# Kernel tuning notes

Measured on AMD Instinct MI355X. Metric: run time of the kernel, lower is better.

Reference implementation:

```python
import jax, jax.numpy as jnp
from jax import lax
import numpy as np

CH = 512      # ch_in = c_in = c_out
P = 8         # p: channels per group
NG = CH // P  # depthwise groups
PG = CH // P  # pointwise groups
EPS = 1e-5
DN = ('NCHW', 'OIHW', 'NCHW')


def leaky(x):
    return jnp.where(x >= 0, x, 0.01 * x)  # LeakyReLU default slope


def setup_inputs() -> dict:
    key = jax.random.key(0)
    ks = jax.random.split(key, 8)
    N, H, W = 16, 64, 64
    return {
        'style_encoding': jax.random.normal(ks[0], (N, 512, 4, 4), jnp.float32),
        'content_in': jax.random.normal(ks[1], (N, CH, H, W), jnp.float32),
        'dw_w': jax.random.normal(ks[2], (P, 512, 2, 2), jnp.float32) * 0.05,
        'dw_b': jax.random.normal(ks[3], (P,), jnp.float32) * 0.05,
        'pk_w': jax.random.normal(ks[4], (P, 512), jnp.float32) * 0.05,
        'pk_b': jax.random.normal(ks[5], (P,), jnp.float32) * 0.05,
        'pb_w': jax.random.normal(ks[6], (CH, 512), jnp.float32) * 0.05,
        'pb_b': jax.random.normal(ks[7], (CH,), jnp.float32) * 0.05,
    }


def reference(style_encoding, content_in, dw_w, dw_b, pk_w, pk_b, pb_w, pb_b):
    N, _, H, W = content_in.shape
    # --- KernelPredictor ---
    # depthwise kernels: 2x2 valid conv on 4x4 style map -> [N, P, 3, 3]
    d = lax.conv_general_dilated(style_encoding, dw_w, (1, 1), 'VALID',
                                 dimension_numbers=DN)
    d = leaky(d + dw_b[None, :, None, None])  # [N, P, 3, 3]
    # expand: same [P,3,3] filter for every output channel -> [N, CH, P, 3, 3]
    depthwise = jnp.broadcast_to(d[:, None], (N, CH, P, 3, 3))
    # avg-pool 4 on 4x4 style map == global mean -> [N, 512]
    s_d = jnp.mean(style_encoding, axis=(2, 3))
    pk = jnp.einsum('nc,oc->no', s_d, pk_w) + pk_b       # [N, P]  (1x1 conv)
    bias = jnp.einsum('nc,oc->no', s_d, pb_w) + pb_b     # [N, CH] (1x1 conv)

    # --- per-sample grouped convs, batched by folding batch into groups ---
    padded = jnp.pad(content_in, ((0, 0), (0, 0), (1, 1), (1, 1)), mode='reflect')
    xr = padded.reshape(1, N * CH, H + 2, W + 2)
    wr = depthwise.reshape(N * CH, P, 3, 3)
    depth = lax.conv_general_dilated(xr, wr, (1, 1), 'VALID',
                                     feature_group_count=N * NG,
                                     dimension_numbers=DN)
    depth = depth.reshape(N, CH, H, W)

    # pointwise 1x1 grouped conv: weight [N, CH, P, 1, 1], identical over out
    # channels within a sample (expand); groups = PG, CH//PG == P out ch/group
    depth_g = depth.reshape(N, PG, P, H, W)
    pw_g = jnp.broadcast_to(pk[:, None, None, :], (N, PG, P, P))  # [n,g,o,j]
    out = jnp.einsum('ngjhw,ngoj->ngohw', depth_g, pw_g).reshape(N, CH, H, W)
    predicted = leaky(out + bias[:, :, None, None])

    # --- instance-norm of content (AdaIN calc_mean_std, unbiased var) ---
    mean = jnp.mean(content_in, axis=(2, 3), keepdims=True)
    std = jnp.sqrt(jnp.var(content_in, axis=(2, 3), keepdims=True, ddof=1) + EPS)
    normalized = (content_in - mean) / std
    return normalized * predicted
```

## Files before the change

### kernel.cpp

```cpp
#include <hip/hip_runtime.h>
#include <math.h>

#define CH 512
#define P 8
#define PLANE 4096
#define EPS 1e-5f

__device__ __forceinline__ float leaky(float x) { return x >= 0.f ? x : 0.01f * x; }

__device__ __forceinline__ float wave_sum(float v) {
    #pragma unroll
    for (int off = 32; off; off >>= 1) v += __shfl_xor(v, off, 64);
    return v;
}

__global__ __launch_bounds__(64) void sd_pk_kernel(
    const float* __restrict__ style,
    const float* __restrict__ pk_w,
    const float* __restrict__ pk_b,
    float* __restrict__ sd_out,
    float* __restrict__ S_out)
{
    const int n = blockIdx.x;
    const int lane = threadIdx.x;
    const float4* sp = (const float4*)(style + (size_t)n * 8192);
    float sd[8];
    #pragma unroll
    for (int i = 0; i < 8; ++i) {
        int c = lane + 64 * i;
        float4 a = sp[c * 4 + 0], b = sp[c * 4 + 1];
        float4 d = sp[c * 4 + 2], e = sp[c * 4 + 3];
        float s = a.x + a.y + a.z + a.w + b.x + b.y + b.z + b.w
                + d.x + d.y + d.z + d.w + e.x + e.y + e.z + e.w;
        sd[i] = s * (1.f / 16.f);
        sd_out[n * 512 + c] = sd[i];
    }
    float Ssum = 0.f;
    #pragma unroll
    for (int o = 0; o < 8; ++o) {
        float acc = 0.f;
        #pragma unroll
        for (int i = 0; i < 8; ++i)
            acc += pk_w[o * 512 + lane + 64 * i] * sd[i];
        Ssum += wave_sum(acc) + pk_b[o];
    }
    if (lane == 0) S_out[n] = Ssum;
}

__global__ __launch_bounds__(256) void dconv_kernel(
    const float* __restrict__ style,
    const float* __restrict__ dw_w,
    const float* __restrict__ dw_b,
    float* __restrict__ d_pred)
{
    const int W = blockIdx.x * 4 + (threadIdx.x >> 6);
    const int lane = threadIdx.x & 63;
    const int n = W / 72, r = W % 72;
    const int j = r / 9, pos = r % 9, y = pos / 3, x = pos % 3;
    const float* sb = style + (size_t)n * 8192;
    const float4* wp = (const float4*)dw_w;
    float acc = 0.f;
    #pragma unroll
    for (int i = 0; i < 8; ++i) {
        int c = lane + 64 * i;
        float4 w = wp[j * 512 + c];
        const float* s = sb + c * 16 + y * 4 + x;
        acc += s[0] * w.x + s[1] * w.y + s[4] * w.z + s[5] * w.w;
    }
    acc = wave_sum(acc);
    if (lane == 0) d_pred[n * 72 + r] = leaky(acc + dw_b[j]);
}

__global__ __launch_bounds__(256) void bias_kernel(
    const float* __restrict__ sd,
    const float* __restrict__ pb_w,
    const float* __restrict__ pb_b,
    float* __restrict__ bias_out)
{
    const int c = blockIdx.x * 4 + (threadIdx.x >> 6);
    const int lane = threadIdx.x & 63;
    float w[8];
    #pragma unroll
    for (int i = 0; i < 8; ++i) w[i] = pb_w[(size_t)c * 512 + lane + 64 * i];
    float acc[16];
    #pragma unroll
    for (int nn = 0; nn < 16; ++nn) acc[nn] = 0.f;
    #pragma unroll
    for (int i = 0; i < 8; ++i) {
        #pragma unroll
        for (int nn = 0; nn < 16; ++nn)
            acc[nn] += w[i] * sd[nn * 512 + lane + 64 * i];
    }
    #pragma unroll
    for (int nn = 0; nn < 16; ++nn) acc[nn] = wave_sum(acc[nn]);
    if (lane == 0) {
        float bb = pb_b[c];
        #pragma unroll
        for (int nn = 0; nn < 16; ++nn) bias_out[nn * 512 + c] = acc[nn] + bb;
    }
}

__global__ __launch_bounds__(256) void stats_kernel(
    const float* __restrict__ content,
    float* __restrict__ mean_out,
    float* __restrict__ rstd_out)
{
    const int nc = blockIdx.x;
    const int t = threadIdx.x;
    const float4* base = (const float4*)(content + (size_t)nc * PLANE);
    float s = 0.f, sq = 0.f;
    #pragma unroll
    for (int k = 0; k < 4; ++k) {
        float4 v = base[k * 256 + t];
        s  += v.x + v.y + v.z + v.w;
        sq += v.x * v.x + v.y * v.y + v.z * v.z + v.w * v.w;
    }
    #pragma unroll
    for (int off = 32; off > 0; off >>= 1) {
        s  += __shfl_down(s, off, 64);
        sq += __shfl_down(sq, off, 64);
    }
    __shared__ float ls[4], lq[4];
    const int wave = t >> 6, lane = t & 63;
    if (lane == 0) { ls[wave] = s; lq[wave] = sq; }
    __syncthreads();
    if (t == 0) {
        float S = ls[0] + ls[1] + ls[2] + ls[3];
        float Q = lq[0] + lq[1] + lq[2] + lq[3];
        float m = S * (1.f / 4096.f);
        float var = (Q - 4096.f * m * m) * (1.f / 4095.f);
        mean_out[nc] = m;
        rstd_out[nc] = rsqrtf(var + EPS);
    }
}

__global__ __launch_bounds__(256) void main_kernel(
    const float* __restrict__ content,
    const float* __restrict__ d_pred,
    const float* __restrict__ S_in,
    const float* __restrict__ bias_in,
    const float* __restrict__ mean_in,
    const float* __restrict__ rstd_in,
    float* __restrict__ out)
{
    const int b    = blockIdx.x;
    const int tile = b & 3;
    const int g    = (b >> 2) & 63;
    const int n    = b >> 8;
    const int t  = threadIdx.x;
    const int tx = t & 15, ty = t >> 4;
    const int h  = tile * 16 + ty;
    const int x0 = tx * 4;

    __shared__ float s_d[72];
    __shared__ float s_S;
    __shared__ float s_bias[8], s_mean[8], s_rstd[8];
    if (t < 72) s_d[t] = d_pred[n * 72 + t];
    if (t == 80) s_S = S_in[n];
    if (t >= 88 && t < 96) {
        int o = t - 88;
        int c = n * 512 + g * 8 + o;
        s_bias[o] = bias_in[c];
        s_mean[o] = mean_in[c];
        s_rstd[o] = rstd_in[c];
    }
    __syncthreads();

    const float* cbase = content + (size_t)(n * 512 + g * 8) * PLANE;
    float D0 = 0.f, D1 = 0.f, D2 = 0.f, D3 = 0.f;
    float4 xc[8];

    #pragma unroll
    for (int j = 0; j < 8; ++j) {
        const float* cj = cbase + j * PLANE;
        #pragma unroll
        for (int r = 0; r < 3; ++r) {
            int y = h - 1 + r;
            int ry = y < 0 ? 1 : (y > 63 ? 62 : y);
            float4 v = *(const float4*)(cj + ry * 64 + x0);
            float lv = __shfl_up(v.w, 1, 64);
            float rv = __shfl_down(v.x, 1, 64);
            float xm = (tx == 0)  ? v.y : lv;
            float xp = (tx == 15) ? v.z : rv;
            const float w0 = s_d[j * 9 + r * 3 + 0];
            const float w1 = s_d[j * 9 + r * 3 + 1];
            const float w2 = s_d[j * 9 + r * 3 + 2];
            D0 += w0 * xm  + w1 * v.x + w2 * v.y;
            D1 += w0 * v.x + w1 * v.y + w2 * v.z;
            D2 += w0 * v.y + w1 * v.z + w2 * v.w;
            D3 += w0 * v.z + w1 * v.w + w2 * xp;
            if (r == 1) xc[j] = v;
        }
    }

    const float S = s_S;
    const float P0 = D0 * S, P1 = D1 * S, P2 = D2 * S, P3 = D3 * S;
    float* obase = out + (size_t)(n * 512 + g * 8) * PLANE + h * 64 + x0;
    #pragma unroll
    for (int o = 0; o < 8; ++o) {
        float bb = s_bias[o], m = s_mean[o], rs = s_rstd[o];
        float4 res;
        res.x = (xc[o].x - m) * rs * leaky(P0 + bb);
        res.y = (xc[o].y - m) * rs * leaky(P1 + bb);
        res.z = (xc[o].z - m) * rs * leaky(P2 + bb);
        res.w = (xc[o].w - m) * rs * leaky(P3 + bb);
        *(float4*)(obase + o * PLANE) = res;
    }
}

extern "C" void kernel_launch(void* const* d_in, const int* in_sizes, int n_in,
                              void* d_out, int out_size, void* d_ws, size_t ws_size,
                              hipStream_t stream) {
    const float* style   = (const float*)d_in[0];
    const float* content = (const float*)d_in[1];
    const float* dw_w    = (const float*)d_in[2];
    const float* dw_b    = (const float*)d_in[3];
    const float* pk_w    = (const float*)d_in[4];
    const float* pk_b    = (const float*)d_in[5];
    const float* pb_w    = (const float*)d_in[6];
    const float* pb_b    = (const float*)d_in[7];
    float* out = (float*)d_out;
    float* ws  = (float*)d_ws;

    const int N = 16;
    float* sd_ws   = ws;
    float* d_pred  = sd_ws + N * 512;
    float* S_ws    = d_pred + N * 72;
    float* bias_ws = S_ws + N;
    float* mean_ws = bias_ws + N * 512;
    float* rstd_ws = mean_ws + N * 512;

    sd_pk_kernel<<<N, 64, 0, stream>>>(style, pk_w, pk_b, sd_ws, S_ws);
    dconv_kernel<<<N * 72 / 4, 256, 0, stream>>>(style, dw_w, dw_b, d_pred);
    bias_kernel<<<512 / 4, 256, 0, stream>>>(sd_ws, pb_w, pb_b, bias_ws);
    stats_kernel<<<N * 512, 256, 0, stream>>>(content, mean_ws, rstd_ws);
    main_kernel<<<N * 64 * 4, 256, 0, stream>>>(content, d_pred, S_ws, bias_ws,
                                                mean_ws, rstd_ws, out);
}
```

Baseline: 278.5 us.

## Fuse instance-norm stats and bias GEMV into main kernel, merge style kernels

After: 309.2 us. +11.0%, slower.

```diff
diff --git a/kernel.cpp b/kernel.cpp
--- a/kernel.cpp
+++ b/kernel.cpp
@@ -1,10 +1,10 @@
 #include <hip/hip_runtime.h>
 #include <math.h>
 
-#define CH 512
-#define P 8
 #define PLANE 4096
 #define EPS 1e-5f
+
+typedef float f4 __attribute__((ext_vector_type(4)));
 
 __device__ __forceinline__ float leaky(float x) { return x >= 0.f ? x : 0.01f * x; }
 
@@ -14,197 +14,176 @@
     return v;
 }
 
-__global__ __launch_bounds__(64) void sd_pk_kernel(
+__global__ __launch_bounds__(256) void style_kernel(
     const float* __restrict__ style,
+    const float* __restrict__ dw_w,
+    const float* __restrict__ dw_b,
     const float* __restrict__ pk_w,
     const float* __restrict__ pk_b,
     float* __restrict__ sd_out,
-    float* __restrict__ S_out)
-{
-    const int n = blockIdx.x;
-    const int lane = threadIdx.x;
-    const float4* sp = (const float4*)(style + (size_t)n * 8192);
-    float sd[8];
-    #pragma unroll
-    for (int i = 0; i < 8; ++i) {
-        int c = lane + 64 * i;
-        float4 a = sp[c * 4 + 0], b = sp[c * 4 + 1];
-        float4 d = sp[c * 4 + 2], e = sp[c * 4 + 3];
-        float s = a.x + a.y + a.z + a.w + b.x + b.y + b.z + b.w
-                + d.x + d.y + d.z + d.w + e.x + e.y + e.z + e.w;
-        sd[i] = s * (1.f / 16.f);
-        sd_out[n * 512 + c] = sd[i];
-    }
-    float Ssum = 0.f;
-    #pragma unroll
-    for (int o = 0; o < 8; ++o) {
-        float acc = 0.f;
-        #pragma unroll
-        for (int i = 0; i < 8; ++i)
-            acc += pk_w[o * 512 + lane + 64 * i] * sd[i];
-        Ssum += wave_sum(acc) + pk_b[o];
-    }
-    if (lane == 0) S_out[n] = Ssum;
-}
-
-__global__ __launch_bounds__(256) void dconv_kernel(
-    const float* __restrict__ style,
-    const float* __restrict__ dw_w,
-    const float* __restrict__ dw_b,
+    float* __restrict__ S_out,
     float* __restrict__ d_pred)
 {
-    const int W = blockIdx.x * 4 + (threadIdx.x >> 6);
-    const int lane = threadIdx.x & 63;
-    const int n = W / 72, r = W % 72;
-    const int j = r / 9, pos = r % 9, y = pos / 3, x = pos % 3;
+    const int blk = blockIdx.x;
+    const int n = blk & 15;
+    const int t = threadIdx.x;
+    const int wave = t >> 6, lane = t & 63;
     const float* sb = style + (size_t)n * 8192;
-    const float4* wp = (const float4*)dw_w;
-    float acc = 0.f;
-    #pragma unroll
-    for (int i = 0; i < 8; ++i) {
-        int c = lane + 64 * i;
-        float4 w = wp[j * 512 + c];
-        const float* s = sb + c * 16 + y * 4 + x;
-        acc += s[0] * w.x + s[1] * w.y + s[4] * w.z + s[5] * w.w;
-    }
-    acc = wave_sum(acc);
-    if (lane == 0) d_pred[n * 72 + r] = leaky(acc + dw_b[j]);
-}
-
-__global__ __launch_bounds__(256) void bias_kernel(
+
+    if (blk < 16) {
+        __shared__ float s_sd[512];
+        __shared__ float red[4];
+        #pragma unroll
+        for (int q = 0; q < 2; ++q) {
+            int c = t + 256 * q;
+            const float4* sp = (const float4*)sb + c * 4;
+            float4 a = sp[0], b = sp[1], d = sp[2], e = sp[3];
+            float s = a.x + a.y + a.z + a.w + b.x + b.y + b.z + b.w
+                    + d.x + d.y + d.z + d.w + e.x + e.y + e.z + e.w;
+            s *= (1.f / 16.f);
+            s_sd[c] = s;
+            sd_out[n * 512 + c] = s;
+        }
+        __syncthreads();
+        float part = 0.f;
+        #pragma unroll
+        for (int o = 0; o < 8; ++o)
+            part += pk_w[o * 512 + t] * s_sd[t]
+                  + pk_w[o * 512 + t + 256] * s_sd[t + 256];
+        part = wave_sum(part);
+        if (lane == 0) red[wave] = part;
+        __syncthreads();
+        if (t == 0) {
+            float S = red[0] + red[1] + red[2] + red[3];
+            #pragma unroll
+            for (int o = 0; o < 8; ++o) S += pk_b[o];
+            S_out[n] = S;
+        }
+    } else {
+        const float4* wp = (const float4*)dw_w;
+        for (int rr = 0; rr < 18; ++rr) {
+            int r = wave * 18 + rr;
+            int j = r / 9, pos = r % 9, y = pos / 3, x = pos % 3;
+            float acc = 0.f;
+            #pragma unroll
+            for (int i = 0; i < 8; ++i) {
+                int c = lane + 64 * i;
+                float4 w = wp[j * 512 + c];
+                const float* s = sb + c * 16 + y * 4 + x;
+                acc += s[0] * w.x + s[1] * w.y + s[4] * w.z + s[5] * w.w;
+            }
+            acc = wave_sum(acc);
+            if (lane == 0) d_pred[n * 72 + r] = leaky(acc + dw_b[j]);
+        }
+    }
+}
+
+__global__ __launch_bounds__(256) void fused_kernel(
+    const float* __restrict__ content,
+    const float* __restrict__ d_pred,
+    const float* __restrict__ S_in,
     const float* __restrict__ sd,
     const float* __restrict__ pb_w,
     const float* __restrict__ pb_b,
-    float* __restrict__ bias_out)
-{
-    const int c = blockIdx.x * 4 + (threadIdx.x >> 6);
-    const int lane = threadIdx.x & 63;
-    float w[8];
-    #pragma unroll
-    for (int i = 0; i < 8; ++i) w[i] = pb_w[(size_t)c * 512 + lane + 64 * i];
-    float acc[16];
-    #pragma unroll
-    for (int nn = 0; nn < 16; ++nn) acc[nn] = 0.f;
-    #pragma unroll
-    for (int i = 0; i < 8; ++i) {
-        #pragma unroll
-        for (int nn = 0; nn < 16; ++nn)
-            acc[nn] += w[i] * sd[nn * 512 + lane + 64 * i];
-    }
-    #pragma unroll
-    for (int nn = 0; nn < 16; ++nn) acc[nn] = wave_sum(acc[nn]);
-    if (lane == 0) {
-        float bb = pb_b[c];
-        #pragma unroll
-        for (int nn = 0; nn < 16; ++nn) bias_out[nn * 512 + c] = acc[nn] + bb;
-    }
-}
-
-__global__ __launch_bounds__(256) void stats_kernel(
-    const float* __restrict__ content,
-    float* __restrict__ mean_out,
-    float* __restrict__ rstd_out)
-{
-    const int nc = blockIdx.x;
-    const int t = threadIdx.x;
-    const float4* base = (const float4*)(content + (size_t)nc * PLANE);
-    float s = 0.f, sq = 0.f;
-    #pragma unroll
-    for (int k = 0; k < 4; ++k) {
-        float4 v = base[k * 256 + t];
-        s  += v.x + v.y + v.z + v.w;
-        sq += v.x * v.x + v.y * v.y + v.z * v.z + v.w * v.w;
-    }
-    #pragma unroll
-    for (int off = 32; off > 0; off >>= 1) {
-        s  += __shfl_down(s, off, 64);
-        sq += __shfl_down(sq, off, 64);
-    }
-    __shared__ float ls[4], lq[4];
-    const int wave = t >> 6, lane = t & 63;
-    if (lane == 0) { ls[wave] = s; lq[wave] = sq; }
-    __syncthreads();
-    if (t == 0) {
-        float S = ls[0] + ls[1] + ls[2] + ls[3];
-        float Q = lq[0] + lq[1] + lq[2] + lq[3];
-        float m = S * (1.f / 4096.f);
-        float var = (Q - 4096.f * m * m) * (1.f / 4095.f);
-        mean_out[nc] = m;
-        rstd_out[nc] = rsqrtf(var + EPS);
-    }
-}
-
-__global__ __launch_bounds__(256) void main_kernel(
-    const float* __restrict__ content,
-    const float* __restrict__ d_pred,
-    const float* __restrict__ S_in,
-    const float* __restrict__ bias_in,
-    const float* __restrict__ mean_in,
-    const float* __restrict__ rstd_in,
     float* __restrict__ out)
 {
-    const int b    = blockIdx.x;
-    const int tile = b & 3;
-    const int g    = (b >> 2) & 63;
-    const int n    = b >> 8;
-    const int t  = threadIdx.x;
+    const int b = blockIdx.x;
+    const int g = b & 63, n = b >> 6;
+    const int t = threadIdx.x;
     const int tx = t & 15, ty = t >> 4;
-    const int h  = tile * 16 + ty;
-    const int x0 = tx * 4;
+    const int wave = t >> 6, lane = t & 63;
 
     __shared__ float s_d[72];
     __shared__ float s_S;
     __shared__ float s_bias[8], s_mean[8], s_rstd[8];
+    __shared__ float reds[32], redq[32];
+
     if (t < 72) s_d[t] = d_pred[n * 72 + t];
     if (t == 80) s_S = S_in[n];
-    if (t >= 88 && t < 96) {
-        int o = t - 88;
-        int c = n * 512 + g * 8 + o;
-        s_bias[o] = bias_in[c];
-        s_mean[o] = mean_in[c];
-        s_rstd[o] = rstd_in[c];
-    }
-    __syncthreads();
+
+    {
+        const int o = t >> 5, l = t & 31;
+        const float* pw  = pb_w + (size_t)(g * 8 + o) * 512;
+        const float* sdn = sd + n * 512;
+        float acc = 0.f;
+        #pragma unroll
+        for (int i = 0; i < 16; ++i) acc += pw[l + 32 * i] * sdn[l + 32 * i];
+        #pragma unroll
+        for (int off = 16; off; off >>= 1) acc += __shfl_xor(acc, off, 64);
+        if (l == 0) s_bias[o] = acc + pb_b[g * 8 + o];
+    }
 
     const float* cbase = content + (size_t)(n * 512 + g * 8) * PLANE;
-    float D0 = 0.f, D1 = 0.f, D2 = 0.f, D3 = 0.f;
-    float4 xc[8];
 
     #pragma unroll
     for (int j = 0; j < 8; ++j) {
-        const float* cj = cbase + j * PLANE;
-        #pragma unroll
-        for (int r = 0; r < 3; ++r) {
-            int y = h - 1 + r;
-            int ry = y < 0 ? 1 : (y > 63 ? 62 : y);
-            float4 v = *(const float4*)(cj + ry * 64 + x0);
-            float lv = __shfl_up(v.w, 1, 64);
-            float rv = __shfl_down(v.x, 1, 64);
-            float xm = (tx == 0)  ? v.y : lv;
-            float xp = (tx == 15) ? v.z : rv;
-            const float w0 = s_d[j * 9 + r * 3 + 0];
-            const float w1 = s_d[j * 9 + r * 3 + 1];
-            const float w2 = s_d[j * 9 + r * 3 + 2];
-            D0 += w0 * xm  + w1 * v.x + w2 * v.y;
-            D1 += w0 * v.x + w1 * v.y + w2 * v.z;
-            D2 += w0 * v.y + w1 * v.z + w2 * v.w;
-            D3 += w0 * v.z + w1 * v.w + w2 * xp;
-            if (r == 1) xc[j] = v;
-        }
-    }
+        const float4* p = (const float4*)(cbase + j * PLANE);
+        float sm = 0.f, sq = 0.f;
+        #pragma unroll
+        for (int k = 0; k < 4; ++k) {
+            float4 v = p[k * 256 + t];
+            sm += v.x + v.y + v.z + v.w;
+            sq += v.x * v.x + v.y * v.y + v.z * v.z + v.w * v.w;
+        }
+        #pragma unroll
+        for (int off = 32; off; off >>= 1) {
+            sm += __shfl_xor(sm, off, 64);
+            sq += __shfl_xor(sq, off, 64);
+        }
+        if (lane == 0) { reds[j * 4 + wave] = sm; redq[j * 4 + wave] = sq; }
+    }
+    __syncthreads();
+    if (t < 8) {
+        float S4 = reds[t * 4] + reds[t * 4 + 1] + reds[t * 4 + 2] + reds[t * 4 + 3];
+        float Q4 = redq[t * 4] + redq[t * 4 + 1] + redq[t * 4 + 2] + redq[t * 4 + 3];
+        float m = S4 * (1.f / 4096.f);
+        float var = (Q4 - 4096.f * m * m) * (1.f / 4095.f);
+        s_mean[t] = m;
+        s_rstd[t] = rsqrtf(var + EPS);
+    }
+    __syncthreads();
 
     const float S = s_S;
-    const float P0 = D0 * S, P1 = D1 * S, P2 = D2 * S, P3 = D3 * S;
-    float* obase = out + (size_t)(n * 512 + g * 8) * PLANE + h * 64 + x0;
-    #pragma unroll
-    for (int o = 0; o < 8; ++o) {
-        float bb = s_bias[o], m = s_mean[o], rs = s_rstd[o];
-        float4 res;
-        res.x = (xc[o].x - m) * rs * leaky(P0 + bb);
-        res.y = (xc[o].y - m) * rs * leaky(P1 + bb);
-        res.z = (xc[o].z - m) * rs * leaky(P2 + bb);
-        res.w = (xc[o].w - m) * rs * leaky(P3 + bb);
-        *(float4*)(obase + o * PLANE) = res;
+    #pragma unroll 1
+    for (int k = 0; k < 4; ++k) {
+        const int h = k * 16 + ty;
+        const int x0 = tx * 4;
+        float D0 = 0.f, D1 = 0.f, D2 = 0.f, D3 = 0.f;
+        float4 xc[8];
+        #pragma unroll
+        for (int j = 0; j < 8; ++j) {
+            const float* cj = cbase + j * PLANE;
+            #pragma unroll
+            for (int r = 0; r < 3; ++r) {
+                int y = h - 1 + r;
+                int ry = y < 0 ? 1 : (y > 63 ? 62 : y);
+                float4 v = *(const float4*)(cj + ry * 64 + x0);
+                float lv = __shfl_up(v.w, 1, 64);
+                float rv = __shfl_down(v.x, 1, 64);
+                float xm = (tx == 0)  ? v.y : lv;
+                float xp = (tx == 15) ? v.z : rv;
+                const float w0 = s_d[j * 9 + r * 3 + 0];
+                const float w1 = s_d[j * 9 + r * 3 + 1];
+                const float w2 = s_d[j * 9 + r * 3 + 2];
+                D0 += w0 * xm  + w1 * v.x + w2 * v.y;
+                D1 += w0 * v.x + w1 * v.y + w2 * v.z;
+                D2 += w0 * v.y + w1 * v.z + w2 * v.w;
+                D3 += w0 * v.z + w1 * v.w + w2 * xp;
+                if (r == 1) xc[j] = v;
+            }
+        }
+        const float P0 = D0 * S, P1 = D1 * S, P2 = D2 * S, P3 = D3 * S;
+        float* obase = out + (size_t)(n * 512 + g * 8) * PLANE + h * 64 + x0;
+        #pragma unroll
+        for (int o = 0; o < 8; ++o) {
+            float bb = s_bias[o], m = s_mean[o], rs = s_rstd[o];
+            f4 res;
+            res.x = (xc[o].x - m) * rs * leaky(P0 + bb);
+            res.y = (xc[o].y - m) * rs * leaky(P1 + bb);
+            res.z = (xc[o].z - m) * rs * leaky(P2 + bb);
+            res.w = (xc[o].w - m) * rs * leaky(P3 + bb);
+            __builtin_nontemporal_store(res, (f4*)(obase + o * PLANE));
+        }
     }
 }
 
@@ -223,17 +202,12 @@
     float* ws  = (float*)d_ws;
 
     const int N = 16;
-    float* sd_ws   = ws;
-    float* d_pred  = sd_ws + N * 512;
-    float* S_ws    = d_pred + N * 72;
-    float* bias_ws = S_ws + N;
-    float* mean_ws = bias_ws + N * 512;
-    float* rstd_ws = mean_ws + N * 512;
-
-    sd_pk_kernel<<<N, 64, 0, stream>>>(style, pk_w, pk_b, sd_ws, S_ws);
-    dconv_kernel<<<N * 72 / 4, 256, 0, stream>>>(style, dw_w, dw_b, d_pred);
-    bias_kernel<<<512 / 4, 256, 0, stream>>>(sd_ws, pb_w, pb_b, bias_ws);
-    stats_kernel<<<N * 512, 256, 0, stream>>>(content, mean_ws, rstd_ws);
-    main_kernel<<<N * 64 * 4, 256, 0, stream>>>(content, d_pred, S_ws, bias_ws,
-                                                mean_ws, rstd_ws, out);
-}
+    float* sd_ws  = ws;
+    float* d_pred = sd_ws + N * 512;
+    float* S_ws   = d_pred + N * 72;
+
+    style_kernel<<<32, 256, 0, stream>>>(style, dw_w, dw_b, pk_w, pk_b,
+                                         sd_ws, S_ws, d_pred);
+    fused_kernel<<<N * 64, 256, 0, stream>>>(content, d_pred, S_ws, sd_ws,
+                                             pb_w, pb_b, out);
+}
```

## Stage content halo tiles in LDS in two four-channel phases

Applied to the files above, without the earlier changes.

Measured after the change: 353.6 us. 26.9% more time.

```diff
diff --git a/kernel.cpp b/kernel.cpp
--- a/kernel.cpp
+++ b/kernel.cpp
@@ -5,6 +5,12 @@
 #define P 8
 #define PLANE 4096
 #define EPS 1e-5f
+
+#define ROWS 18
+#define LDW  68
+#define LPLANE (ROWS * LDW)
+
+typedef float f4 __attribute__((ext_vector_type(4)));
 
 __device__ __forceinline__ float leaky(float x) { return x >= 0.f ? x : 0.01f * x; }
 
@@ -134,7 +140,7 @@
     }
 }
 
-__global__ __launch_bounds__(256) void main_kernel(
+__global__ __launch_bounds__(256, 6) void main_kernel(
     const float* __restrict__ content,
     const float* __restrict__ d_pred,
     const float* __restrict__ S_in,
@@ -152,9 +158,11 @@
     const int h  = tile * 16 + ty;
     const int x0 = tx * 4;
 
+    __shared__ float s_x[4 * LPLANE];
     __shared__ float s_d[72];
     __shared__ float s_S;
     __shared__ float s_bias[8], s_mean[8], s_rstd[8];
+
     if (t < 72) s_d[t] = d_pred[n * 72 + t];
     if (t == 80) s_S = S_in[n];
     if (t >= 88 && t < 96) {
@@ -164,24 +172,39 @@
         s_mean[o] = mean_in[c];
         s_rstd[o] = rstd_in[c];
     }
+
+    const float* cbase = content + (size_t)(n * 512 + g * 8) * PLANE;
+    const int xmi = (tx == 0)  ? 1  : x0 - 1;
+    const int xpi = (tx == 15) ? 62 : x0 + 4;
+
+    float D0 = 0.f, D1 = 0.f, D2 = 0.f, D3 = 0.f;
+    f4 xc0[4];
+
+    #pragma unroll
+    for (int i = 0; i < 5; ++i) {
+        int q = t + 256 * i;
+        if (q < 1152) {
+            int p   = q / 288;
+            int rem = q - p * 288;
+            int row = rem >> 4;
+            int c4  = rem & 15;
+            int y   = tile * 16 + row - 1;
+            int ry  = y < 0 ? 1 : (y > 63 ? 62 : y);
+            f4 v = *(const f4*)(cbase + p * PLANE + ry * 64 + c4 * 4);
+            *(f4*)(s_x + p * LPLANE + row * LDW + c4 * 4) = v;
+        }
+    }
     __syncthreads();
 
-    const float* cbase = content + (size_t)(n * 512 + g * 8) * PLANE;
-    float D0 = 0.f, D1 = 0.f, D2 = 0.f, D3 = 0.f;
-    float4 xc[8];
-
-    #pragma unroll
-    for (int j = 0; j < 8; ++j) {
-        const float* cj = cbase + j * PLANE;
+    #pragma unroll
+    for (int j = 0; j < 4; ++j) {
+        const float* base = s_x + j * LPLANE;
         #pragma unroll
         for (int r = 0; r < 3; ++r) {
-            int y = h - 1 + r;
-            int ry = y < 0 ? 1 : (y > 63 ? 62 : y);
-            float4 v = *(const float4*)(cj + ry * 64 + x0);
-            float lv = __shfl_up(v.w, 1, 64);
-            float rv = __shfl_down(v.x, 1, 64);
-            float xm = (tx == 0)  ? v.y : lv;
-            float xp = (tx == 15) ? v.z : rv;
+            const float* rowp = base + (ty + r) * LDW;
+            f4 v = *(const f4*)(rowp + x0);
+            float xm = rowp[xmi];
+            float xp = rowp[xpi];
             const float w0 = s_d[j * 9 + r * 3 + 0];
             const float w1 = s_d[j * 9 + r * 3 + 1];
             const float w2 = s_d[j * 9 + r * 3 + 2];
@@ -189,7 +212,43 @@
             D1 += w0 * v.x + w1 * v.y + w2 * v.z;
             D2 += w0 * v.y + w1 * v.z + w2 * v.w;
             D3 += w0 * v.z + w1 * v.w + w2 * xp;
-            if (r == 1) xc[j] = v;
+        }
+        xc0[j] = *(const f4*)(base + (ty + 1) * LDW + x0);
+    }
+    __syncthreads();
+
+    #pragma unroll
+    for (int i = 0; i < 5; ++i) {
+        int q = t + 256 * i;
+        if (q < 1152) {
+            int p   = q / 288;
+            int rem = q - p * 288;
+            int row = rem >> 4;
+            int c4  = rem & 15;
+            int y   = tile * 16 + row - 1;
+            int ry  = y < 0 ? 1 : (y > 63 ? 62 : y);
+            f4 v = *(const f4*)(cbase + (p + 4) * PLANE + ry * 64 + c4 * 4);
+            *(f4*)(s_x + p * LPLANE + row * LDW + c4 * 4) = v;
+        }
+    }
+    __syncthreads();
+
+    #pragma unroll
+    for (int j = 0; j < 4; ++j) {
+        const float* base = s_x + j * LPLANE;
+        #pragma unroll
+        for (int r = 0; r < 3; ++r) {
+            const float* rowp = base + (ty + r) * LDW;
+            f4 v = *(const f4*)(rowp + x0);
+            float xm = rowp[xmi];
+            float xp = rowp[xpi];
+            const float w0 = s_d[(j + 4) * 9 + r * 3 + 0];
+            const float w1 = s_d[(j + 4) * 9 + r * 3 + 1];
+            const float w2 = s_d[(j + 4) * 9 + r * 3 + 2];
+            D0 += w0 * xm  + w1 * v.x + w2 * v.y;
+            D1 += w0 * v.x + w1 * v.y + w2 * v.z;
+            D2 += w0 * v.y + w1 * v.z + w2 * v.w;
+            D3 += w0 * v.z + w1 * v.w + w2 * xp;
         }
     }
 
@@ -197,14 +256,26 @@
     const float P0 = D0 * S, P1 = D1 * S, P2 = D2 * S, P3 = D3 * S;
     float* obase = out + (size_t)(n * 512 + g * 8) * PLANE + h * 64 + x0;
     #pragma unroll
-    for (int o = 0; o < 8; ++o) {
+    for (int o = 0; o < 4; ++o) {
+        f4 v = xc0[o];
         float bb = s_bias[o], m = s_mean[o], rs = s_rstd[o];
-        float4 res;
-        res.x = (xc[o].x - m) * rs * leaky(P0 + bb);
-        res.y = (xc[o].y - m) * rs * leaky(P1 + bb);
-        res.z = (xc[o].z - m) * rs * leaky(P2 + bb);
-        res.w = (xc[o].w - m) * rs * leaky(P3 + bb);
-        *(float4*)(obase + o * PLANE) = res;
+        f4 res;
+        res.x = (v.x - m) * rs * leaky(P0 + bb);
+        res.y = (v.y - m) * rs * leaky(P1 + bb);
+        res.z = (v.z - m) * rs * leaky(P2 + bb);
+        res.w = (v.w - m) * rs * leaky(P3 + bb);
+        *(f4*)(obase + o * PLANE) = res;
+    }
+    #pragma unroll
+    for (int o = 4; o < 8; ++o) {
+        f4 v = *(const f4*)(s_x + (o - 4) * LPLANE + (ty + 1) * LDW + x0);
+        float bb = s_bias[o], m = s_mean[o], rs = s_rstd[o];
+        f4 res;
+        res.x = (v.x - m) * rs * leaky(P0 + bb);
+        res.y = (v.y - m) * rs * leaky(P1 + bb);
+        res.z = (v.z - m) * rs * leaky(P2 + bb);
+        res.w = (v.w - m) * rs * leaky(P3 + bb);
+        *(f4*)(obase + o * PLANE) = res;
     }
 }
 
```
